# Kernel optimization log

Hardware: AMD Instinct MI355X
Metric: run time of the kernel (lower is better)

Reference implementation:

```python
import jax, jax.numpy as jnp
import numpy as np

D, H, E, TAU = 1024, 2048, 8, 0.1
X_SHAPE = (2, 2048, D)
N = X_SHAPE[0] * X_SHAPE[1]


def setup_inputs() -> dict:
    key = jax.random.key(0)
    ks = jax.random.split(key, 12)
    s_in = 1.0 / np.sqrt(D)
    s_hid = 1.0 / np.sqrt(H)
    return {
        "x": jax.random.normal(ks[0], X_SHAPE, jnp.float32),
        "gumbel_u": jax.random.uniform(ks[1], (N, E), jnp.float32, 1e-6, 1.0 - 1e-6),
        "eps": jax.random.normal(ks[2], (N, E, D), jnp.float32),
        "Wg1": jax.random.normal(ks[3], (D, H), jnp.float32) * s_in,
        "bg1": jnp.zeros((H,), jnp.float32),
        "Wg2": jax.random.normal(ks[4], (H, E), jnp.float32) * s_hid,
        "bg2": jnp.zeros((E,), jnp.float32),
        "Wm1": jax.random.normal(ks[5], (E, D, H), jnp.float32) * s_in,
        "bm1": jnp.zeros((E, H), jnp.float32),
        "Wm2": jax.random.normal(ks[6], (E, H, D), jnp.float32) * s_hid,
        "bm2": jnp.zeros((E, D), jnp.float32),
        "Wv1": jax.random.normal(ks[7], (E, D, H), jnp.float32) * s_in,
        "bv1": jnp.zeros((E, H), jnp.float32),
        "Wv2": jax.random.normal(ks[8], (E, H, D), jnp.float32) * s_hid,
        "bv2": jnp.zeros((E, D), jnp.float32),
    }


def reference(x, gumbel_u, eps, Wg1, bg1, Wg2, bg2, Wm1, bm1, Wm2, bm2, Wv1, bv1, Wv2, bv2):
    orig_shape = x.shape
    xf = x.reshape(-1, D)  # [N, D]

    # Gate: Linear -> ReLU -> Linear, then soft Gumbel-Softmax
    gate_logits = jax.nn.relu(xf @ Wg1 + bg1) @ Wg2 + bg2  # [N, E]
    gumbel = -jnp.log(-jnp.log(gumbel_u))
    w = jax.nn.softmax((gate_logits + gumbel) / TAU, axis=-1)  # [N, E]

    # Per-expert 2-layer MLPs, batched over the expert axis as grouped GEMMs
    hm = jax.nn.relu(jnp.einsum("nd,edh->neh", xf, Wm1) + bm1)
    mus = jnp.einsum("neh,ehd->ned", hm, Wm2) + bm2  # [N, E, D]
    hv = jax.nn.relu(jnp.einsum("nd,edh->neh", xf, Wv1) + bv1)
    logvars = jnp.einsum("neh,ehd->ned", hv, Wv2) + bv2  # [N, E, D]

    # Reparameterized sample per expert, then gate-weighted sum over experts
    samples = mus + eps * jnp.exp(0.5 * logvars)  # [N, E, D]
    out = jnp.einsum("ne,ned->nd", w, samples)  # [N, D]
    return out.reshape(orig_shape)
```

## Files before the change

kernel.cpp:

```cpp
#include <hip/hip_runtime.h>


typedef _Float16 f16x8 __attribute__((ext_vector_type(8)));
typedef float    f32x4 __attribute__((ext_vector_type(4)));

__device__ __forceinline__ void async_copy16(const void* g, void* l) {
  __builtin_amdgcn_global_load_lds(
      (const __attribute__((address_space(1))) void*)g,
      (__attribute__((address_space(3))) void*)l, 16, 0, 0);
}


__global__ __launch_bounds__(256) void split_x_kernel(
    const float* __restrict__ x, _Float16* __restrict__ Ax) {
  int idx = blockIdx.x * 256 + threadIdx.x;
  int m = idx >> 10, k = idx & 1023;
  float v = x[idx];
  _Float16 hi = (_Float16)v;
  _Float16 lo = (_Float16)(v - (float)hi);
  _Float16* row = Ax + (size_t)m * 3072;
  row[k] = hi;
  row[k + 1024] = hi;
  row[k + 2048] = lo;
}

__global__ __launch_bounds__(256) void split_transpose_wg1_kernel(
    const float* __restrict__ in, _Float16* __restrict__ out) {
  __shared__ float tile[64][65];
  int kb = blockIdx.y * 64, nb = blockIdx.x * 64;
  int c = threadIdx.x & 63, r0 = threadIdx.x >> 6;
#pragma unroll
  for (int i = 0; i < 16; ++i) {
    int r = r0 + i * 4;
    tile[r][c] = in[(size_t)(kb + r) * 2048 + nb + c];
  }
  __syncthreads();
#pragma unroll
  for (int i = 0; i < 16; ++i) {
    int rn = r0 + i * 4;
    float v = tile[c][rn];
    _Float16 hi = (_Float16)v;
    _Float16 lo = (_Float16)(v - (float)hi);
    _Float16* row = out + (size_t)(nb + rn) * 3072 + kb;
    row[c] = hi;
    row[c + 1024] = lo;
    row[c + 2048] = hi;
  }
}

__global__ __launch_bounds__(256) void transpose_f32_to_f16(
    const float* __restrict__ in, _Float16* __restrict__ out, int K, int N) {
  __shared__ float tile[64][65];
  size_t zo = (size_t)blockIdx.z * K * N;
  int kb = blockIdx.y * 64, nb = blockIdx.x * 64;
  int c = threadIdx.x & 63, r0 = threadIdx.x >> 6;
  const float* ip = in + zo + (size_t)kb * N + nb;
#pragma unroll
  for (int i = 0; i < 16; ++i) {
    int r = r0 + i * 4;
    tile[r][c] = ip[(size_t)r * N + c];
  }
  __syncthreads();
  _Float16* op = out + zo + (size_t)nb * K + kb;
#pragma unroll
  for (int i = 0; i < 16; ++i) {
    int rn = r0 + i * 4;
    op[(size_t)rn * K + c] = (_Float16)tile[c][rn];
  }
}

__global__ __launch_bounds__(256) void zero_out_kernel(float4* __restrict__ p) {
  p[blockIdx.x * 256 + threadIdx.x] = float4{0.f, 0.f, 0.f, 0.f};
}

__global__ __launch_bounds__(256) void gate_gemm1_kernel(
    const _Float16* __restrict__ A, const _Float16* __restrict__ Bt,
    float* __restrict__ C, const float* __restrict__ bias) {
  __shared__ _Float16 As[128 * 32];
  __shared__ _Float16 Bs[128 * 32];
  const int tid = threadIdx.x, lane = tid & 63, wid = tid >> 6;
  const int m0 = blockIdx.y * 128, n0 = blockIdx.x * 128;
  const int wm = (wid >> 1) * 64, wn = (wid & 1) * 64;
  const int lanelo = lane & 15, laneq = lane >> 4;
  const int K = 3072, lda = 3072, ldc = 2048;
  f32x4 acc[4][4] = {};

  const int c0 = wid * 128 + lane, c1 = c0 + 64;
  const int ra0 = c0 >> 2, ca0 = (c0 & 3) * 8;
  const int ra1 = c1 >> 2, ca1 = (c1 & 3) * 8;
  _Float16* ldsA0 = As + (wid * 128 + 0) * 8;
  _Float16* ldsA1 = As + (wid * 128 + 64) * 8;
  _Float16* ldsB0 = Bs + (wid * 128 + 0) * 8;
  _Float16* ldsB1 = Bs + (wid * 128 + 64) * 8;
  const _Float16* Arow0 = A + (size_t)(m0 + ra0) * lda + ca0;
  const _Float16* Arow1 = A + (size_t)(m0 + ra1) * lda + ca1;
  const _Float16* Brow0 = Bt + (size_t)(n0 + ra0) * K + ca0;
  const _Float16* Brow1 = Bt + (size_t)(n0 + ra1) * K + ca1;

  for (int k0 = 0; k0 < K; k0 += 32) {
    async_copy16(Arow0 + k0, ldsA0);
    async_copy16(Arow1 + k0, ldsA1);
    async_copy16(Brow0 + k0, ldsB0);
    async_copy16(Brow1 + k0, ldsB1);
    __syncthreads();
    f16x8 a[4], b[4];
#pragma unroll
    for (int i = 0; i < 4; ++i)
      a[i] = *reinterpret_cast<const f16x8*>(
          &As[(wm + i * 16 + lanelo) * 32 + laneq * 8]);
#pragma unroll
    for (int j = 0; j < 4; ++j)
      b[j] = *reinterpret_cast<const f16x8*>(
          &Bs[(wn + j * 16 + lanelo) * 32 + laneq * 8]);
#pragma unroll
    for (int i = 0; i < 4; ++i)
#pragma unroll
      for (int j = 0; j < 4; ++j)
        acc[i][j] =
            __builtin_amdgcn_mfma_f32_16x16x32_f16(a[i], b[j], acc[i][j], 0, 0, 0);
    __syncthreads();
  }

#pragma unroll
  for (int j = 0; j < 4; ++j) {
    const int n = n0 + wn + j * 16 + lanelo;
    const float bn = bias[n];
#pragma unroll
    for (int i = 0; i < 4; ++i) {
#pragma unroll
      for (int r = 0; r < 4; ++r) {
        const int m = m0 + wm + i * 16 + laneq * 4 + r;
        float v = acc[i][j][r] + bn;
        C[(size_t)m * ldc + n] = v > 0.f ? v : 0.f;
      }
    }
  }
}

__global__ __launch_bounds__(256) void expert_gemm1_kernel(
    const _Float16* __restrict__ A, const _Float16* __restrict__ W1t,
    _Float16* __restrict__ hm, _Float16* __restrict__ hv,
    const float* __restrict__ bm1, const float* __restrict__ bv1) {
  __shared__ _Float16 As[128 * 32];
  __shared__ _Float16 Bs[128 * 32];
  const int tid = threadIdx.x, lane = tid & 63, wid = tid >> 6;
  const int s = blockIdx.z & 1, e = blockIdx.z >> 1;
  const _Float16* __restrict__ Bt = W1t + (size_t)(s * 8 + e) * 2048 * 1024;
  _Float16* __restrict__ C = (s ? hv : hm) + (size_t)e * 4096 * 2048;
  const float* __restrict__ bias = (s ? bv1 : bm1) + e * 2048;
  const int m0 = blockIdx.y * 128, n0 = blockIdx.x * 128;
  const int wm = (wid >> 1) * 64, wn = (wid & 1) * 64;
  const int lanelo = lane & 15, laneq = lane >> 4;
  const int K = 1024, lda = 3072, ldc = 2048;
  f32x4 acc[4][4] = {};

  const int c0 = wid * 128 + lane, c1 = c0 + 64;
  const int ra0 = c0 >> 2, ca0 = (c0 & 3) * 8;
  const int ra1 = c1 >> 2, ca1 = (c1 & 3) * 8;
  _Float16* ldsA0 = As + (wid * 128 + 0) * 8;
  _Float16* ldsA1 = As + (wid * 128 + 64) * 8;
  _Float16* ldsB0 = Bs + (wid * 128 + 0) * 8;
  _Float16* ldsB1 = Bs + (wid * 128 + 64) * 8;
  const _Float16* Arow0 = A + (size_t)(m0 + ra0) * lda + ca0;
  const _Float16* Arow1 = A + (size_t)(m0 + ra1) * lda + ca1;
  const _Float16* Brow0 = Bt + (size_t)(n0 + ra0) * K + ca0;
  const _Float16* Brow1 = Bt + (size_t)(n0 + ra1) * K + ca1;

  for (int k0 = 0; k0 < K; k0 += 32) {
    async_copy16(Arow0 + k0, ldsA0);
    async_copy16(Arow1 + k0, ldsA1);
    async_copy16(Brow0 + k0, ldsB0);
    async_copy16(Brow1 + k0, ldsB1);
    __syncthreads();
    f16x8 a[4], b[4];
#pragma unroll
    for (int i = 0; i < 4; ++i)
      a[i] = *reinterpret_cast<const f16x8*>(
          &As[(wm + i * 16 + lanelo) * 32 + laneq * 8]);
#pragma unroll
    for (int j = 0; j < 4; ++j)
      b[j] = *reinterpret_cast<const f16x8*>(
          &Bs[(wn + j * 16 + lanelo) * 32 + laneq * 8]);
#pragma unroll
    for (int i = 0; i < 4; ++i)
#pragma unroll
      for (int j = 0; j < 4; ++j)
        acc[i][j] =
            __builtin_amdgcn_mfma_f32_16x16x32_f16(a[i], b[j], acc[i][j], 0, 0, 0);
    __syncthreads();
  }

#pragma unroll
  for (int j = 0; j < 4; ++j) {
    const int n = n0 + wn + j * 16 + lanelo;
    const float bn = bias[n];
#pragma unroll
    for (int i = 0; i < 4; ++i) {
#pragma unroll
      for (int r = 0; r < 4; ++r) {
        const int m = m0 + wm + i * 16 + laneq * 4 + r;
        float v = acc[i][j][r] + bn;
        C[(size_t)m * ldc + n] = (_Float16)(v > 0.f ? v : 0.f);
      }
    }
  }
}

__global__ __launch_bounds__(256) void gemm2_combine_kernel(
    const _Float16* __restrict__ hm, const _Float16* __restrict__ hv,
    const _Float16* __restrict__ W2t, const float* __restrict__ bm2,
    const float* __restrict__ bv2, const float* __restrict__ eps,
    const float* __restrict__ w, float* __restrict__ out) {
  __shared__ _Float16 As[128 * 32];
  __shared__ _Float16 Bs[128 * 32];
  const int tid = threadIdx.x, lane = tid & 63, wid = tid >> 6;
  const int s = blockIdx.z & 1, e = blockIdx.z >> 1;
  const _Float16* __restrict__ A = (s ? hv : hm) + (size_t)e * 4096 * 2048;
  const _Float16* __restrict__ Bt = W2t + (size_t)(s * 8 + e) * 1024 * 2048;
  const float* __restrict__ bias = (s ? bv2 : bm2) + e * 1024;
  const float* __restrict__ epsE = eps + e * 1024;
  const int m0 = blockIdx.y * 128, n0 = blockIdx.x * 128;
  const int wm = (wid >> 1) * 64, wn = (wid & 1) * 64;
  const int lanelo = lane & 15, laneq = lane >> 4;
  const int K = 2048, lda = 2048;
  f32x4 acc[4][4] = {};

  const int c0 = wid * 128 + lane, c1 = c0 + 64;
  const int ra0 = c0 >> 2, ca0 = (c0 & 3) * 8;
  const int ra1 = c1 >> 2, ca1 = (c1 & 3) * 8;
  _Float16* ldsA0 = As + (wid * 128 + 0) * 8;
  _Float16* ldsA1 = As + (wid * 128 + 64) * 8;
  _Float16* ldsB0 = Bs + (wid * 128 + 0) * 8;
  _Float16* ldsB1 = Bs + (wid * 128 + 64) * 8;
  const _Float16* Arow0 = A + (size_t)(m0 + ra0) * lda + ca0;
  const _Float16* Arow1 = A + (size_t)(m0 + ra1) * lda + ca1;
  const _Float16* Brow0 = Bt + (size_t)(n0 + ra0) * K + ca0;
  const _Float16* Brow1 = Bt + (size_t)(n0 + ra1) * K + ca1;

  for (int k0 = 0; k0 < K; k0 += 32) {
    async_copy16(Arow0 + k0, ldsA0);
    async_copy16(Arow1 + k0, ldsA1);
    async_copy16(Brow0 + k0, ldsB0);
    async_copy16(Brow1 + k0, ldsB1);
    __syncthreads();
    f16x8 a[4], b[4];
#pragma unroll
    for (int i = 0; i < 4; ++i)
      a[i] = *reinterpret_cast<const f16x8*>(
          &As[(wm + i * 16 + lanelo) * 32 + laneq * 8]);
#pragma unroll
    for (int j = 0; j < 4; ++j)
      b[j] = *reinterpret_cast<const f16x8*>(
          &Bs[(wn + j * 16 + lanelo) * 32 + laneq * 8]);
#pragma unroll
    for (int i = 0; i < 4; ++i)
#pragma unroll
      for (int j = 0; j < 4; ++j)
        acc[i][j] =
            __builtin_amdgcn_mfma_f32_16x16x32_f16(a[i], b[j], acc[i][j], 0, 0, 0);
    __syncthreads();
  }

#pragma unroll
  for (int i = 0; i < 4; ++i) {
#pragma unroll
    for (int r = 0; r < 4; ++r) {
      const int m = m0 + wm + i * 16 + laneq * 4 + r;
      const float wgt = w[(size_t)m * 8 + e];
      const float* erow = epsE + (size_t)m * 8192;
      float* orow = out + (size_t)m * 1024;
#pragma unroll
      for (int j = 0; j < 4; ++j) {
        const int d = n0 + wn + j * 16 + lanelo;
        const float t = acc[i][j][r] + bias[d];
        const float val =
            s ? wgt * erow[d] * __expf(0.5f * t) : wgt * t;
        unsafeAtomicAdd(&orow[d], val);
      }
    }
  }
}

__global__ __launch_bounds__(256) void gate_finish_kernel(
    const float* __restrict__ hg, const float* __restrict__ Wg2,
    const float* __restrict__ bg2, const float* __restrict__ gu,
    float* __restrict__ w) {
  const int lane = threadIdx.x & 63, wid = threadIdx.x >> 6;
  const int row = blockIdx.x * 4 + wid;
  const float* hrow = hg + (size_t)row * 2048;
  float acc[8] = {0.f, 0.f, 0.f, 0.f, 0.f, 0.f, 0.f, 0.f};
  for (int h = lane; h < 2048; h += 64) {
    const float hv = hrow[h];
    const float* wr = Wg2 + (size_t)h * 8;
#pragma unroll
    for (int e = 0; e < 8; ++e) acc[e] += hv * wr[e];
  }
#pragma unroll
  for (int off = 32; off > 0; off >>= 1) {
#pragma unroll
    for (int e = 0; e < 8; ++e) acc[e] += __shfl_down(acc[e], off);
  }
  if (lane == 0) {
    float z[8], zmax = -1e30f;
#pragma unroll
    for (int e = 0; e < 8; ++e) {
      const float u = gu[(size_t)row * 8 + e];
      const float g = -logf(-logf(u));
      z[e] = (acc[e] + bg2[e] + g) / 0.1f;
      zmax = fmaxf(zmax, z[e]);
    }
    float s = 0.f;
#pragma unroll
    for (int e = 0; e < 8; ++e) {
      z[e] = __expf(z[e] - zmax);
      s += z[e];
    }
    const float inv = 1.f / s;
#pragma unroll
    for (int e = 0; e < 8; ++e) w[(size_t)row * 8 + e] = z[e] * inv;
  }
}


extern "C" void kernel_launch(void* const* d_in, const int* in_sizes, int n_in,
                              void* d_out, int out_size, void* d_ws,
                              size_t ws_size, hipStream_t stream) {
  const float* x = (const float*)d_in[0];
  const float* gu = (const float*)d_in[1];
  const float* eps = (const float*)d_in[2];
  const float* Wg1 = (const float*)d_in[3];
  const float* bg1 = (const float*)d_in[4];
  const float* Wg2 = (const float*)d_in[5];
  const float* bg2 = (const float*)d_in[6];
  const float* Wm1 = (const float*)d_in[7];
  const float* bm1 = (const float*)d_in[8];
  const float* Wm2 = (const float*)d_in[9];
  const float* bm2 = (const float*)d_in[10];
  const float* Wv1 = (const float*)d_in[11];
  const float* bv1 = (const float*)d_in[12];
  const float* Wv2 = (const float*)d_in[13];
  const float* bv2 = (const float*)d_in[14];
  float* out = (float*)d_out;

  char* ws = (char*)d_ws;
  size_t off = 0;
  auto alloc = [&](size_t bytes) -> void* {
    void* p = ws + off;
    off = (off + bytes + 255) & ~(size_t)255;
    return p;
  };
  _Float16* Ax = (_Float16*)alloc(4096UL * 3072 * 2);
  _Float16* Wg1t = (_Float16*)alloc(2048UL * 3072 * 2);
  _Float16* W1t = (_Float16*)alloc(16UL * 2048 * 1024 * 2);
  _Float16* W2t = (_Float16*)alloc(16UL * 1024 * 2048 * 2);
  float* hg = (float*)alloc(4096UL * 2048 * 4);
  float* wbuf = (float*)alloc(4096UL * 8 * 4);
  _Float16* hm = (_Float16*)alloc(8UL * 4096 * 2048 * 2);
  _Float16* hv = (_Float16*)alloc(8UL * 4096 * 2048 * 2);

  zero_out_kernel<<<4096, 256, 0, stream>>>((float4*)out);
  split_x_kernel<<<4096 * 1024 / 256, 256, 0, stream>>>(x, Ax);
  split_transpose_wg1_kernel<<<dim3(2048 / 64, 1024 / 64), 256, 0, stream>>>(Wg1, Wg1t);
  transpose_f32_to_f16<<<dim3(2048 / 64, 1024 / 64, 8), 256, 0, stream>>>(
      Wm1, W1t, 1024, 2048);
  transpose_f32_to_f16<<<dim3(2048 / 64, 1024 / 64, 8), 256, 0, stream>>>(
      Wv1, W1t + 8UL * 2048 * 1024, 1024, 2048);
  transpose_f32_to_f16<<<dim3(1024 / 64, 2048 / 64, 8), 256, 0, stream>>>(
      Wm2, W2t, 2048, 1024);
  transpose_f32_to_f16<<<dim3(1024 / 64, 2048 / 64, 8), 256, 0, stream>>>(
      Wv2, W2t + 8UL * 1024 * 2048, 2048, 1024);

  gate_gemm1_kernel<<<dim3(2048 / 128, 4096 / 128), 256, 0, stream>>>(
      Ax, Wg1t, hg, bg1);
  gate_finish_kernel<<<4096 / 4, 256, 0, stream>>>(hg, Wg2, bg2, gu, wbuf);

  expert_gemm1_kernel<<<dim3(2048 / 128, 4096 / 128, 16), 256, 0, stream>>>(
      Ax, W1t, hm, hv, bm1, bv1);
  gemm2_combine_kernel<<<dim3(1024 / 128, 4096 / 128, 16), 256, 0, stream>>>(
      hm, hv, W2t, bm2, bv2, eps, wbuf, out);
}
```

Baseline: 1.410 ms.

## Fuse mu/logvar expert GEMMs to share A tiles and halve output atomics

Expert GEMM1 now computes both the mu and logvar hidden tiles in one block, loading the shared x tile once and keeping two accumulator sets. GEMM2 runs the logvar GEMM first, folds eps*exp(0.5*logvar)+mu-bias into the accumulator, then continues accumulating the mu GEMM on top, so each output element gets a single atomic add per expert instead of two. The LDS write offsets are also simplified to c0*8. This cuts A-tile traffic and atomics at the cost of higher register pressure (two accumulator sets, launch_bounds 256,2) and half as many blocks per launch.

```diff
diff --git a/kernel.cpp b/kernel.cpp
--- a/kernel.cpp
+++ b/kernel.cpp
@@ -88,10 +88,10 @@
   const int c0 = wid * 128 + lane, c1 = c0 + 64;
   const int ra0 = c0 >> 2, ca0 = (c0 & 3) * 8;
   const int ra1 = c1 >> 2, ca1 = (c1 & 3) * 8;
-  _Float16* ldsA0 = As + (wid * 128 + 0) * 8;
-  _Float16* ldsA1 = As + (wid * 128 + 64) * 8;
-  _Float16* ldsB0 = Bs + (wid * 128 + 0) * 8;
-  _Float16* ldsB1 = Bs + (wid * 128 + 64) * 8;
+  _Float16* ldsA0 = As + c0 * 8;
+  _Float16* ldsA1 = As + c1 * 8;
+  _Float16* ldsB0 = Bs + c0 * 8;
+  _Float16* ldsB1 = Bs + c1 * 8;
   const _Float16* Arow0 = A + (size_t)(m0 + ra0) * lda + ca0;
   const _Float16* Arow1 = A + (size_t)(m0 + ra1) * lda + ca1;
   const _Float16* Brow0 = Bt + (size_t)(n0 + ra0) * K + ca0;
@@ -137,40 +137,51 @@
   }
 }
 
-__global__ __launch_bounds__(256) void expert_gemm1_kernel(
+__global__ __launch_bounds__(256, 2) void expert_gemm1_kernel(
     const _Float16* __restrict__ A, const _Float16* __restrict__ W1t,
     _Float16* __restrict__ hm, _Float16* __restrict__ hv,
     const float* __restrict__ bm1, const float* __restrict__ bv1) {
   __shared__ _Float16 As[128 * 32];
-  __shared__ _Float16 Bs[128 * 32];
+  __shared__ _Float16 Bms[128 * 32];
+  __shared__ _Float16 Bvs[128 * 32];
   const int tid = threadIdx.x, lane = tid & 63, wid = tid >> 6;
-  const int s = blockIdx.z & 1, e = blockIdx.z >> 1;
-  const _Float16* __restrict__ Bt = W1t + (size_t)(s * 8 + e) * 2048 * 1024;
-  _Float16* __restrict__ C = (s ? hv : hm) + (size_t)e * 4096 * 2048;
-  const float* __restrict__ bias = (s ? bv1 : bm1) + e * 2048;
+  const int e = blockIdx.z;
+  const _Float16* __restrict__ Btm = W1t + (size_t)e * 2048 * 1024;
+  const _Float16* __restrict__ Btv = W1t + (size_t)(8 + e) * 2048 * 1024;
+  _Float16* __restrict__ Cm = hm + (size_t)e * 4096 * 2048;
+  _Float16* __restrict__ Cv = hv + (size_t)e * 4096 * 2048;
+  const float* __restrict__ bm = bm1 + e * 2048;
+  const float* __restrict__ bv = bv1 + e * 2048;
   const int m0 = blockIdx.y * 128, n0 = blockIdx.x * 128;
   const int wm = (wid >> 1) * 64, wn = (wid & 1) * 64;
   const int lanelo = lane & 15, laneq = lane >> 4;
   const int K = 1024, lda = 3072, ldc = 2048;
-  f32x4 acc[4][4] = {};
+  f32x4 accm[4][4] = {};
+  f32x4 accv[4][4] = {};
 
   const int c0 = wid * 128 + lane, c1 = c0 + 64;
   const int ra0 = c0 >> 2, ca0 = (c0 & 3) * 8;
   const int ra1 = c1 >> 2, ca1 = (c1 & 3) * 8;
-  _Float16* ldsA0 = As + (wid * 128 + 0) * 8;
-  _Float16* ldsA1 = As + (wid * 128 + 64) * 8;
-  _Float16* ldsB0 = Bs + (wid * 128 + 0) * 8;
-  _Float16* ldsB1 = Bs + (wid * 128 + 64) * 8;
+  _Float16* ldsA0 = As + c0 * 8;
+  _Float16* ldsA1 = As + c1 * 8;
+  _Float16* ldsBm0 = Bms + c0 * 8;
+  _Float16* ldsBm1 = Bms + c1 * 8;
+  _Float16* ldsBv0 = Bvs + c0 * 8;
+  _Float16* ldsBv1 = Bvs + c1 * 8;
   const _Float16* Arow0 = A + (size_t)(m0 + ra0) * lda + ca0;
   const _Float16* Arow1 = A + (size_t)(m0 + ra1) * lda + ca1;
-  const _Float16* Brow0 = Bt + (size_t)(n0 + ra0) * K + ca0;
-  const _Float16* Brow1 = Bt + (size_t)(n0 + ra1) * K + ca1;
+  const _Float16* Bmrow0 = Btm + (size_t)(n0 + ra0) * K + ca0;
+  const _Float16* Bmrow1 = Btm + (size_t)(n0 + ra1) * K + ca1;
+  const _Float16* Bvrow0 = Btv + (size_t)(n0 + ra0) * K + ca0;
+  const _Float16* Bvrow1 = Btv + (size_t)(n0 + ra1) * K + ca1;
 
   for (int k0 = 0; k0 < K; k0 += 32) {
     async_copy16(Arow0 + k0, ldsA0);
     async_copy16(Arow1 + k0, ldsA1);
-    async_copy16(Brow0 + k0, ldsB0);
-    async_copy16(Brow1 + k0, ldsB1);
+    async_copy16(Bmrow0 + k0, ldsBm0);
+    async_copy16(Bmrow1 + k0, ldsBm1);
+    async_copy16(Bvrow0 + k0, ldsBv0);
+    async_copy16(Bvrow1 + k0, ldsBv1);
     __syncthreads();
     f16x8 a[4], b[4];
 #pragma unroll
@@ -180,27 +191,39 @@
 #pragma unroll
     for (int j = 0; j < 4; ++j)
       b[j] = *reinterpret_cast<const f16x8*>(
-          &Bs[(wn + j * 16 + lanelo) * 32 + laneq * 8]);
+          &Bms[(wn + j * 16 + lanelo) * 32 + laneq * 8]);
 #pragma unroll
     for (int i = 0; i < 4; ++i)
 #pragma unroll
       for (int j = 0; j < 4; ++j)
-        acc[i][j] =
-            __builtin_amdgcn_mfma_f32_16x16x32_f16(a[i], b[j], acc[i][j], 0, 0, 0);
+        accm[i][j] =
+            __builtin_amdgcn_mfma_f32_16x16x32_f16(a[i], b[j], accm[i][j], 0, 0, 0);
+#pragma unroll
+    for (int j = 0; j < 4; ++j)
+      b[j] = *reinterpret_cast<const f16x8*>(
+          &Bvs[(wn + j * 16 + lanelo) * 32 + laneq * 8]);
+#pragma unroll
+    for (int i = 0; i < 4; ++i)
+#pragma unroll
+      for (int j = 0; j < 4; ++j)
+        accv[i][j] =
+            __builtin_amdgcn_mfma_f32_16x16x32_f16(a[i], b[j], accv[i][j], 0, 0, 0);
     __syncthreads();
   }
 
 #pragma unroll
   for (int j = 0; j < 4; ++j) {
     const int n = n0 + wn + j * 16 + lanelo;
-    const float bn = bias[n];
+    const float bmn = bm[n], bvn = bv[n];
 #pragma unroll
     for (int i = 0; i < 4; ++i) {
 #pragma unroll
       for (int r = 0; r < 4; ++r) {
         const int m = m0 + wm + i * 16 + laneq * 4 + r;
-        float v = acc[i][j][r] + bn;
-        C[(size_t)m * ldc + n] = (_Float16)(v > 0.f ? v : 0.f);
+        float vm = accm[i][j][r] + bmn;
+        float vv = accv[i][j][r] + bvn;
+        Cm[(size_t)m * ldc + n] = (_Float16)(vm > 0.f ? vm : 0.f);
+        Cv[(size_t)m * ldc + n] = (_Float16)(vv > 0.f ? vv : 0.f);
       }
     }
   }
@@ -214,11 +237,13 @@
   __shared__ _Float16 As[128 * 32];
   __shared__ _Float16 Bs[128 * 32];
   const int tid = threadIdx.x, lane = tid & 63, wid = tid >> 6;
-  const int s = blockIdx.z & 1, e = blockIdx.z >> 1;
-  const _Float16* __restrict__ A = (s ? hv : hm) + (size_t)e * 4096 * 2048;
-  const _Float16* __restrict__ Bt = W2t + (size_t)(s * 8 + e) * 1024 * 2048;
-  const float* __restrict__ bias = (s ? bv2 : bm2) + e * 1024;
-  const float* __restrict__ epsE = eps + e * 1024;
+  const int e = blockIdx.z;
+  const _Float16* __restrict__ Am = hm + (size_t)e * 4096 * 2048;
+  const _Float16* __restrict__ Av = hv + (size_t)e * 4096 * 2048;
+  const _Float16* __restrict__ Btm = W2t + (size_t)e * 1024 * 2048;
+  const _Float16* __restrict__ Btv = W2t + (size_t)(8 + e) * 1024 * 2048;
+  const float* __restrict__ bmb = bm2 + e * 1024;
+  const float* __restrict__ bvb = bv2 + e * 1024;
   const int m0 = blockIdx.y * 128, n0 = blockIdx.x * 128;
   const int wm = (wid >> 1) * 64, wn = (wid & 1) * 64;
   const int lanelo = lane & 15, laneq = lane >> 4;
@@ -228,37 +253,89 @@
   const int c0 = wid * 128 + lane, c1 = c0 + 64;
   const int ra0 = c0 >> 2, ca0 = (c0 & 3) * 8;
   const int ra1 = c1 >> 2, ca1 = (c1 & 3) * 8;
-  _Float16* ldsA0 = As + (wid * 128 + 0) * 8;
-  _Float16* ldsA1 = As + (wid * 128 + 64) * 8;
-  _Float16* ldsB0 = Bs + (wid * 128 + 0) * 8;
-  _Float16* ldsB1 = Bs + (wid * 128 + 64) * 8;
-  const _Float16* Arow0 = A + (size_t)(m0 + ra0) * lda + ca0;
-  const _Float16* Arow1 = A + (size_t)(m0 + ra1) * lda + ca1;
-  const _Float16* Brow0 = Bt + (size_t)(n0 + ra0) * K + ca0;
-  const _Float16* Brow1 = Bt + (size_t)(n0 + ra1) * K + ca1;
-
-  for (int k0 = 0; k0 < K; k0 += 32) {
-    async_copy16(Arow0 + k0, ldsA0);
-    async_copy16(Arow1 + k0, ldsA1);
-    async_copy16(Brow0 + k0, ldsB0);
-    async_copy16(Brow1 + k0, ldsB1);
-    __syncthreads();
-    f16x8 a[4], b[4];
-#pragma unroll
-    for (int i = 0; i < 4; ++i)
-      a[i] = *reinterpret_cast<const f16x8*>(
-          &As[(wm + i * 16 + lanelo) * 32 + laneq * 8]);
-#pragma unroll
-    for (int j = 0; j < 4; ++j)
-      b[j] = *reinterpret_cast<const f16x8*>(
-          &Bs[(wn + j * 16 + lanelo) * 32 + laneq * 8]);
-#pragma unroll
-    for (int i = 0; i < 4; ++i)
+  _Float16* ldsA0 = As + c0 * 8;
+  _Float16* ldsA1 = As + c1 * 8;
+  _Float16* ldsB0 = Bs + c0 * 8;
+  _Float16* ldsB1 = Bs + c1 * 8;
+  const size_t aoff0 = (size_t)(m0 + ra0) * lda + ca0;
+  const size_t aoff1 = (size_t)(m0 + ra1) * lda + ca1;
+  const size_t boff0 = (size_t)(n0 + ra0) * K + ca0;
+  const size_t boff1 = (size_t)(n0 + ra1) * K + ca1;
+
+  {
+    const _Float16* Arow0 = Av + aoff0;
+    const _Float16* Arow1 = Av + aoff1;
+    const _Float16* Brow0 = Btv + boff0;
+    const _Float16* Brow1 = Btv + boff1;
+    for (int k0 = 0; k0 < K; k0 += 32) {
+      async_copy16(Arow0 + k0, ldsA0);
+      async_copy16(Arow1 + k0, ldsA1);
+      async_copy16(Brow0 + k0, ldsB0);
+      async_copy16(Brow1 + k0, ldsB1);
+      __syncthreads();
+      f16x8 a[4], b[4];
+#pragma unroll
+      for (int i = 0; i < 4; ++i)
+        a[i] = *reinterpret_cast<const f16x8*>(
+            &As[(wm + i * 16 + lanelo) * 32 + laneq * 8]);
 #pragma unroll
       for (int j = 0; j < 4; ++j)
-        acc[i][j] =
-            __builtin_amdgcn_mfma_f32_16x16x32_f16(a[i], b[j], acc[i][j], 0, 0, 0);
-    __syncthreads();
+        b[j] = *reinterpret_cast<const f16x8*>(
+            &Bs[(wn + j * 16 + lanelo) * 32 + laneq * 8]);
+#pragma unroll
+      for (int i = 0; i < 4; ++i)
+#pragma unroll
+        for (int j = 0; j < 4; ++j)
+          acc[i][j] =
+              __builtin_amdgcn_mfma_f32_16x16x32_f16(a[i], b[j], acc[i][j], 0, 0, 0);
+      __syncthreads();
+    }
+  }
+
+#pragma unroll
+  for (int j = 0; j < 4; ++j) {
+    const int d = n0 + wn + j * 16 + lanelo;
+    const float bvd = bvb[d];
+    const float bmd = bmb[d];
+#pragma unroll
+    for (int i = 0; i < 4; ++i) {
+#pragma unroll
+      for (int r = 0; r < 4; ++r) {
+        const int m = m0 + wm + i * 16 + laneq * 4 + r;
+        const float ev = eps[(size_t)m * 8192 + e * 1024 + d];
+        acc[i][j][r] = ev * __expf(0.5f * (acc[i][j][r] + bvd)) + bmd;
+      }
+    }
+  }
+
+  {
+    const _Float16* Arow0 = Am + aoff0;
+    const _Float16* Arow1 = Am + aoff1;
+    const _Float16* Brow0 = Btm + boff0;
+    const _Float16* Brow1 = Btm + boff1;
+    for (int k0 = 0; k0 < K; k0 += 32) {
+      async_copy16(Arow0 + k0, ldsA0);
+      async_copy16(Arow1 + k0, ldsA1);
+      async_copy16(Brow0 + k0, ldsB0);
+      async_copy16(Brow1 + k0, ldsB1);
+      __syncthreads();
+      f16x8 a[4], b[4];
+#pragma unroll
+      for (int i = 0; i < 4; ++i)
+        a[i] = *reinterpret_cast<const f16x8*>(
+            &As[(wm + i * 16 + lanelo) * 32 + laneq * 8]);
+#pragma unroll
+      for (int j = 0; j < 4; ++j)
+        b[j] = *reinterpret_cast<const f16x8*>(
+            &Bs[(wn + j * 16 + lanelo) * 32 + laneq * 8]);
+#pragma unroll
+      for (int i = 0; i < 4; ++i)
+#pragma unroll
+        for (int j = 0; j < 4; ++j)
+          acc[i][j] =
+              __builtin_amdgcn_mfma_f32_16x16x32_f16(a[i], b[j], acc[i][j], 0, 0, 0);
+      __syncthreads();
+    }
   }
 
 #pragma unroll
@@ -267,15 +344,11 @@
     for (int r = 0; r < 4; ++r) {
       const int m = m0 + wm + i * 16 + laneq * 4 + r;
       const float wgt = w[(size_t)m * 8 + e];
-      const float* erow = epsE + (size_t)m * 8192;
       float* orow = out + (size_t)m * 1024;
 #pragma unroll
       for (int j = 0; j < 4; ++j) {
         const int d = n0 + wn + j * 16 + lanelo;
-        const float t = acc[i][j][r] + bias[d];
-        const float val =
-            s ? wgt * erow[d] * __expf(0.5f * t) : wgt * t;
-        unsafeAtomicAdd(&orow[d], val);
+        unsafeAtomicAdd(&orow[d], wgt * acc[i][j][r]);
       }
     }
   }
@@ -374,8 +447,8 @@
       Ax, Wg1t, hg, bg1);
   gate_finish_kernel<<<4096 / 4, 256, 0, stream>>>(hg, Wg2, bg2, gu, wbuf);
 
-  expert_gemm1_kernel<<<dim3(2048 / 128, 4096 / 128, 16), 256, 0, stream>>>(
+  expert_gemm1_kernel<<<dim3(2048 / 128, 4096 / 128, 8), 256, 0, stream>>>(
       Ax, W1t, hm, hv, bm1, bv1);
-  gemm2_combine_kernel<<<dim3(1024 / 128, 4096 / 128, 16), 256, 0, stream>>>(
+  gemm2_combine_kernel<<<dim3(1024 / 128, 4096 / 128, 8), 256, 0, stream>>>(
       hm, hv, W2t, bm2, bv2, eps, wbuf, out);
 }
```

New measurement: 1.384 ms. About the same (-1.9%).

## Replace GEMMs with 256x256 double-buffered swizzled MFMA tiles and fuse mu/logvar combine

Applied to the files above, without the earlier changes.

Replaces the three 128x128 single-buffered GEMM kernels with a shared 256x256-tile, 512-thread routine. It uses 128KB of dynamic LDS, double buffering with async global-to-LDS copies, XOR-swizzled layout, split barriers and setprio around the MFMA bursts. The combine kernel now computes the logvar and mu GEMMs for each expert in one block and keeps the sample in registers, which halves the atomic adds to the output. This trades larger tiles and register pressure (two blocks per CU requested) for more data reuse and less LDS stall and atomic traffic.

```diff
diff --git a/kernel.cpp b/kernel.cpp
--- a/kernel.cpp
+++ b/kernel.cpp
@@ -9,6 +9,8 @@
       (const __attribute__((address_space(1))) void*)g,
       (__attribute__((address_space(3))) void*)l, 16, 0, 0);
 }
+
+#define MFMA16(a_, b_, c_) __builtin_amdgcn_mfma_f32_16x16x32_f16(a_, b_, c_, 0, 0, 0)
 
 
 __global__ __launch_bounds__(256) void split_x_kernel(
@@ -73,212 +75,271 @@
   p[blockIdx.x * 256 + threadIdx.x] = float4{0.f, 0.f, 0.f, 0.f};
 }
 
-__global__ __launch_bounds__(256) void gate_gemm1_kernel(
+__device__ __forceinline__ void gemm256_acc(
+    const _Float16* __restrict__ Abase, const int lda,
+    const _Float16* __restrict__ Bbase, const int ldb,
+    const int NT, _Float16* lds, f32x4 (&acc)[8][4]) {
+  const int tid = threadIdx.x;
+  const int lane = tid & 63, wid = tid >> 6;
+  const int wm = wid >> 2, wn = wid & 3;
+  const int lanelo = lane & 15, laneq = lane >> 4;
+  const int colp0 = (laneq * 8) ^ ((lanelo & 7) << 3);
+  const int rowoffA = (wm * 128 + lanelo) * 64;
+  const int rowoffB = (wn * 64 + lanelo) * 64;
+
+  _Float16* const As0 = lds;
+  _Float16* const As1 = lds + 16384;
+  _Float16* const Bs0 = lds + 32768;
+  _Float16* const Bs1 = lds + 49152;
+
+  const int sr = tid >> 3;
+  const int sc = ((tid & 7) ^ (sr & 7)) << 3;
+  const size_t goffA = (size_t)sr * lda + sc;
+  const size_t goffB = (size_t)sr * ldb + sc;
+  const size_t rowsA64 = (size_t)64 * lda;
+  const size_t rowsB64 = (size_t)64 * ldb;
+  const int tid8 = tid * 8;
+
+#define STAGE_A(dstbuf, kp, hf)                                  \
+  do {                                                           \
+    const _Float16* g_ = (kp) + (size_t)(hf)*2 * rowsA64 + goffA;\
+    _Float16* d_ = (dstbuf) + (hf)*8192 + tid8;                  \
+    async_copy16(g_, d_);                                        \
+    async_copy16(g_ + rowsA64, d_ + 4096);                       \
+  } while (0)
+#define STAGE_B(dstbuf, kp, hf)                                  \
+  do {                                                           \
+    const _Float16* g_ = (kp) + (size_t)(hf)*2 * rowsB64 + goffB;\
+    _Float16* d_ = (dstbuf) + (hf)*8192 + tid8;                  \
+    async_copy16(g_, d_);                                        \
+    async_copy16(g_ + rowsB64, d_ + 4096);                       \
+  } while (0)
+#define BARRIER() asm volatile("s_barrier" ::: "memory")
+
+  const _Float16* aN = Abase + 64;
+  const _Float16* bN = Bbase + 128;
+
+  STAGE_A(As0, Abase, 0);
+  STAGE_A(As0, Abase, 1);
+  STAGE_B(Bs0, Bbase, 0);
+  STAGE_B(Bs0, Bbase, 1);
+  STAGE_B(Bs1, Bbase + 64, 0);
+  STAGE_B(Bs1, Bbase + 64, 1);
+  asm volatile("s_waitcnt vmcnt(4)" ::: "memory");
+  BARRIER();
+
+  for (int kt = 0; kt < NT; ++kt) {
+    _Float16* const bufA = (kt & 1) ? As1 : As0;
+    _Float16* const bufB = (kt & 1) ? Bs1 : Bs0;
+    _Float16* const nxtA = (kt & 1) ? As0 : As1;
+    const _Float16* const rA0 = bufA + rowoffA + colp0;
+    const _Float16* const rA1 = bufA + rowoffA + (colp0 ^ 32);
+    const _Float16* const rB0 = bufB + rowoffB + colp0;
+    const _Float16* const rB1 = bufB + rowoffB + (colp0 ^ 32);
+    const bool st1 = (kt + 1 < NT), st2 = (kt + 2 < NT);
+    f16x8 a[4][2], b[4][2];
+
+#pragma unroll
+    for (int i = 0; i < 4; ++i) {
+      a[i][0] = *(const f16x8*)(rA0 + i * 1024);
+      a[i][1] = *(const f16x8*)(rA1 + i * 1024);
+    }
+#pragma unroll
+    for (int j = 0; j < 2; ++j) {
+      b[j][0] = *(const f16x8*)(rB0 + j * 1024);
+      b[j][1] = *(const f16x8*)(rB1 + j * 1024);
+    }
+    if (st1) STAGE_A(nxtA, aN, 0);
+    BARRIER();
+    __builtin_amdgcn_sched_barrier(0);
+    __builtin_amdgcn_s_setprio(1);
+#pragma unroll
+    for (int i = 0; i < 4; ++i)
+#pragma unroll
+      for (int j = 0; j < 2; ++j) {
+        acc[i][j] = MFMA16(a[i][0], b[j][0], acc[i][j]);
+        acc[i][j] = MFMA16(a[i][1], b[j][1], acc[i][j]);
+      }
+    __builtin_amdgcn_s_setprio(0);
+    __builtin_amdgcn_sched_barrier(0);
+    BARRIER();
+
+#pragma unroll
+    for (int j = 0; j < 2; ++j) {
+      b[2 + j][0] = *(const f16x8*)(rB0 + (2 + j) * 1024);
+      b[2 + j][1] = *(const f16x8*)(rB1 + (2 + j) * 1024);
+    }
+    if (st1) STAGE_A(nxtA, aN, 1);
+    BARRIER();
+    __builtin_amdgcn_sched_barrier(0);
+    __builtin_amdgcn_s_setprio(1);
+#pragma unroll
+    for (int i = 0; i < 4; ++i)
+#pragma unroll
+      for (int j = 0; j < 2; ++j) {
+        acc[i][2 + j] = MFMA16(a[i][0], b[2 + j][0], acc[i][2 + j]);
+        acc[i][2 + j] = MFMA16(a[i][1], b[2 + j][1], acc[i][2 + j]);
+      }
+    __builtin_amdgcn_s_setprio(0);
+    __builtin_amdgcn_sched_barrier(0);
+    BARRIER();
+
+#pragma unroll
+    for (int i = 0; i < 4; ++i) {
+      a[i][0] = *(const f16x8*)(rA0 + 4096 + i * 1024);
+      a[i][1] = *(const f16x8*)(rA1 + 4096 + i * 1024);
+    }
+    if (st2) STAGE_B(bufB, bN, 0);
+    BARRIER();
+    __builtin_amdgcn_sched_barrier(0);
+    __builtin_amdgcn_s_setprio(1);
+#pragma unroll
+    for (int i = 0; i < 4; ++i)
+#pragma unroll
+      for (int j = 0; j < 2; ++j) {
+        acc[4 + i][j] = MFMA16(a[i][0], b[j][0], acc[4 + i][j]);
+        acc[4 + i][j] = MFMA16(a[i][1], b[j][1], acc[4 + i][j]);
+      }
+    __builtin_amdgcn_s_setprio(0);
+    __builtin_amdgcn_sched_barrier(0);
+    BARRIER();
+
+    if (st2) STAGE_B(bufB, bN, 1);
+    BARRIER();
+    __builtin_amdgcn_sched_barrier(0);
+    __builtin_amdgcn_s_setprio(1);
+#pragma unroll
+    for (int i = 0; i < 4; ++i)
+#pragma unroll
+      for (int j = 0; j < 2; ++j) {
+        acc[4 + i][2 + j] = MFMA16(a[i][0], b[2 + j][0], acc[4 + i][2 + j]);
+        acc[4 + i][2 + j] = MFMA16(a[i][1], b[2 + j][1], acc[4 + i][2 + j]);
+      }
+    __builtin_amdgcn_s_setprio(0);
+    __builtin_amdgcn_sched_barrier(0);
+    if (st2) {
+      asm volatile("s_waitcnt vmcnt(4)" ::: "memory");
+    } else {
+      asm volatile("s_waitcnt vmcnt(0)" ::: "memory");
+    }
+    BARRIER();
+
+    aN += 64;
+    bN += 64;
+  }
+#undef STAGE_A
+#undef STAGE_B
+#undef BARRIER
+}
+
+__global__ __launch_bounds__(512, 2) void gate_gemm1_256(
     const _Float16* __restrict__ A, const _Float16* __restrict__ Bt,
     float* __restrict__ C, const float* __restrict__ bias) {
-  __shared__ _Float16 As[128 * 32];
-  __shared__ _Float16 Bs[128 * 32];
+  extern __shared__ _Float16 lds[];
+  const int m0 = blockIdx.y * 256, n0 = blockIdx.x * 256;
+  f32x4 acc[8][4] = {};
+  gemm256_acc(A + (size_t)m0 * 3072, 3072, Bt + (size_t)n0 * 3072, 3072, 48,
+              lds, acc);
   const int tid = threadIdx.x, lane = tid & 63, wid = tid >> 6;
-  const int m0 = blockIdx.y * 128, n0 = blockIdx.x * 128;
-  const int wm = (wid >> 1) * 64, wn = (wid & 1) * 64;
+  const int wm = wid >> 2, wn = wid & 3;
   const int lanelo = lane & 15, laneq = lane >> 4;
-  const int K = 3072, lda = 3072, ldc = 2048;
-  f32x4 acc[4][4] = {};
-
-  const int c0 = wid * 128 + lane, c1 = c0 + 64;
-  const int ra0 = c0 >> 2, ca0 = (c0 & 3) * 8;
-  const int ra1 = c1 >> 2, ca1 = (c1 & 3) * 8;
-  _Float16* ldsA0 = As + (wid * 128 + 0) * 8;
-  _Float16* ldsA1 = As + (wid * 128 + 64) * 8;
-  _Float16* ldsB0 = Bs + (wid * 128 + 0) * 8;
-  _Float16* ldsB1 = Bs + (wid * 128 + 64) * 8;
-  const _Float16* Arow0 = A + (size_t)(m0 + ra0) * lda + ca0;
-  const _Float16* Arow1 = A + (size_t)(m0 + ra1) * lda + ca1;
-  const _Float16* Brow0 = Bt + (size_t)(n0 + ra0) * K + ca0;
-  const _Float16* Brow1 = Bt + (size_t)(n0 + ra1) * K + ca1;
-
-  for (int k0 = 0; k0 < K; k0 += 32) {
-    async_copy16(Arow0 + k0, ldsA0);
-    async_copy16(Arow1 + k0, ldsA1);
-    async_copy16(Brow0 + k0, ldsB0);
-    async_copy16(Brow1 + k0, ldsB1);
-    __syncthreads();
-    f16x8 a[4], b[4];
-#pragma unroll
-    for (int i = 0; i < 4; ++i)
-      a[i] = *reinterpret_cast<const f16x8*>(
-          &As[(wm + i * 16 + lanelo) * 32 + laneq * 8]);
-#pragma unroll
-    for (int j = 0; j < 4; ++j)
-      b[j] = *reinterpret_cast<const f16x8*>(
-          &Bs[(wn + j * 16 + lanelo) * 32 + laneq * 8]);
-#pragma unroll
-    for (int i = 0; i < 4; ++i)
-#pragma unroll
-      for (int j = 0; j < 4; ++j)
-        acc[i][j] =
-            __builtin_amdgcn_mfma_f32_16x16x32_f16(a[i], b[j], acc[i][j], 0, 0, 0);
-    __syncthreads();
-  }
-
-#pragma unroll
-  for (int j = 0; j < 4; ++j) {
-    const int n = n0 + wn + j * 16 + lanelo;
+#pragma unroll
+  for (int nf = 0; nf < 4; ++nf) {
+    const int n = n0 + wn * 64 + nf * 16 + lanelo;
     const float bn = bias[n];
 #pragma unroll
-    for (int i = 0; i < 4; ++i) {
+    for (int mf = 0; mf < 8; ++mf)
 #pragma unroll
       for (int r = 0; r < 4; ++r) {
-        const int m = m0 + wm + i * 16 + laneq * 4 + r;
-        float v = acc[i][j][r] + bn;
-        C[(size_t)m * ldc + n] = v > 0.f ? v : 0.f;
-      }
-    }
-  }
-}
-
-__global__ __launch_bounds__(256) void expert_gemm1_kernel(
+        const int m = m0 + wm * 128 + mf * 16 + laneq * 4 + r;
+        float v = acc[mf][nf][r] + bn;
+        C[(size_t)m * 2048 + n] = v > 0.f ? v : 0.f;
+      }
+  }
+}
+
+__global__ __launch_bounds__(512, 2) void expert_gemm1_256(
     const _Float16* __restrict__ A, const _Float16* __restrict__ W1t,
     _Float16* __restrict__ hm, _Float16* __restrict__ hv,
     const float* __restrict__ bm1, const float* __restrict__ bv1) {
-  __shared__ _Float16 As[128 * 32];
-  __shared__ _Float16 Bs[128 * 32];
-  const int tid = threadIdx.x, lane = tid & 63, wid = tid >> 6;
-  const int s = blockIdx.z & 1, e = blockIdx.z >> 1;
-  const _Float16* __restrict__ Bt = W1t + (size_t)(s * 8 + e) * 2048 * 1024;
+  extern __shared__ _Float16 lds[];
+  const int z = blockIdx.z, e = z & 7, s = z >> 3;
+  const _Float16* __restrict__ Bt = W1t + (size_t)z * 2048 * 1024;
   _Float16* __restrict__ C = (s ? hv : hm) + (size_t)e * 4096 * 2048;
   const float* __restrict__ bias = (s ? bv1 : bm1) + e * 2048;
-  const int m0 = blockIdx.y * 128, n0 = blockIdx.x * 128;
-  const int wm = (wid >> 1) * 64, wn = (wid & 1) * 64;
+  const int m0 = blockIdx.y * 256, n0 = blockIdx.x * 256;
+  f32x4 acc[8][4] = {};
+  gemm256_acc(A + (size_t)m0 * 3072, 3072, Bt + (size_t)n0 * 1024, 1024, 16,
+              lds, acc);
+  const int tid = threadIdx.x, lane = tid & 63, wid = tid >> 6;
+  const int wm = wid >> 2, wn = wid & 3;
   const int lanelo = lane & 15, laneq = lane >> 4;
-  const int K = 1024, lda = 3072, ldc = 2048;
-  f32x4 acc[4][4] = {};
-
-  const int c0 = wid * 128 + lane, c1 = c0 + 64;
-  const int ra0 = c0 >> 2, ca0 = (c0 & 3) * 8;
-  const int ra1 = c1 >> 2, ca1 = (c1 & 3) * 8;
-  _Float16* ldsA0 = As + (wid * 128 + 0) * 8;
-  _Float16* ldsA1 = As + (wid * 128 + 64) * 8;
-  _Float16* ldsB0 = Bs + (wid * 128 + 0) * 8;
-  _Float16* ldsB1 = Bs + (wid * 128 + 64) * 8;
-  const _Float16* Arow0 = A + (size_t)(m0 + ra0) * lda + ca0;
-  const _Float16* Arow1 = A + (size_t)(m0 + ra1) * lda + ca1;
-  const _Float16* Brow0 = Bt + (size_t)(n0 + ra0) * K + ca0;
-  const _Float16* Brow1 = Bt + (size_t)(n0 + ra1) * K + ca1;
-
-  for (int k0 = 0; k0 < K; k0 += 32) {
-    async_copy16(Arow0 + k0, ldsA0);
-    async_copy16(Arow1 + k0, ldsA1);
-    async_copy16(Brow0 + k0, ldsB0);
-    async_copy16(Brow1 + k0, ldsB1);
-    __syncthreads();
-    f16x8 a[4], b[4];
-#pragma unroll
-    for (int i = 0; i < 4; ++i)
-      a[i] = *reinterpret_cast<const f16x8*>(
-          &As[(wm + i * 16 + lanelo) * 32 + laneq * 8]);
-#pragma unroll
-    for (int j = 0; j < 4; ++j)
-      b[j] = *reinterpret_cast<const f16x8*>(
-          &Bs[(wn + j * 16 + lanelo) * 32 + laneq * 8]);
-#pragma unroll
-    for (int i = 0; i < 4; ++i)
-#pragma unroll
-      for (int j = 0; j < 4; ++j)
-        acc[i][j] =
-            __builtin_amdgcn_mfma_f32_16x16x32_f16(a[i], b[j], acc[i][j], 0, 0, 0);
-    __syncthreads();
-  }
-
-#pragma unroll
-  for (int j = 0; j < 4; ++j) {
-    const int n = n0 + wn + j * 16 + lanelo;
+#pragma unroll
+  for (int nf = 0; nf < 4; ++nf) {
+    const int n = n0 + wn * 64 + nf * 16 + lanelo;
     const float bn = bias[n];
 #pragma unroll
-    for (int i = 0; i < 4; ++i) {
+    for (int mf = 0; mf < 8; ++mf)
 #pragma unroll
       for (int r = 0; r < 4; ++r) {
-        const int m = m0 + wm + i * 16 + laneq * 4 + r;
-        float v = acc[i][j][r] + bn;
-        C[(size_t)m * ldc + n] = (_Float16)(v > 0.f ? v : 0.f);
-      }
-    }
-  }
-}
-
-__global__ __launch_bounds__(256) void gemm2_combine_kernel(
+        const int m = m0 + wm * 128 + mf * 16 + laneq * 4 + r;
+        float v = acc[mf][nf][r] + bn;
+        C[(size_t)m * 2048 + n] = (_Float16)(v > 0.f ? v : 0.f);
+      }
+  }
+}
+
+__global__ __launch_bounds__(512, 2) void gemm2_combine_256(
     const _Float16* __restrict__ hm, const _Float16* __restrict__ hv,
     const _Float16* __restrict__ W2t, const float* __restrict__ bm2,
     const float* __restrict__ bv2, const float* __restrict__ eps,
     const float* __restrict__ w, float* __restrict__ out) {
-  __shared__ _Float16 As[128 * 32];
-  __shared__ _Float16 Bs[128 * 32];
+  extern __shared__ _Float16 lds[];
+  const int e = blockIdx.z;
+  const _Float16* __restrict__ Am = hm + (size_t)e * 4096 * 2048;
+  const _Float16* __restrict__ Av = hv + (size_t)e * 4096 * 2048;
+  const _Float16* __restrict__ Btm = W2t + (size_t)e * 1024 * 2048;
+  const _Float16* __restrict__ Btv = W2t + (size_t)(8 + e) * 1024 * 2048;
+  const float* __restrict__ bmb = bm2 + e * 1024;
+  const float* __restrict__ bvb = bv2 + e * 1024;
+  const int m0 = blockIdx.y * 256, n0 = blockIdx.x * 256;
   const int tid = threadIdx.x, lane = tid & 63, wid = tid >> 6;
-  const int s = blockIdx.z & 1, e = blockIdx.z >> 1;
-  const _Float16* __restrict__ A = (s ? hv : hm) + (size_t)e * 4096 * 2048;
-  const _Float16* __restrict__ Bt = W2t + (size_t)(s * 8 + e) * 1024 * 2048;
-  const float* __restrict__ bias = (s ? bv2 : bm2) + e * 1024;
-  const float* __restrict__ epsE = eps + e * 1024;
-  const int m0 = blockIdx.y * 128, n0 = blockIdx.x * 128;
-  const int wm = (wid >> 1) * 64, wn = (wid & 1) * 64;
+  const int wm = wid >> 2, wn = wid & 3;
   const int lanelo = lane & 15, laneq = lane >> 4;
-  const int K = 2048, lda = 2048;
-  f32x4 acc[4][4] = {};
-
-  const int c0 = wid * 128 + lane, c1 = c0 + 64;
-  const int ra0 = c0 >> 2, ca0 = (c0 & 3) * 8;
-  const int ra1 = c1 >> 2, ca1 = (c1 & 3) * 8;
-  _Float16* ldsA0 = As + (wid * 128 + 0) * 8;
-  _Float16* ldsA1 = As + (wid * 128 + 64) * 8;
-  _Float16* ldsB0 = Bs + (wid * 128 + 0) * 8;
-  _Float16* ldsB1 = Bs + (wid * 128 + 64) * 8;
-  const _Float16* Arow0 = A + (size_t)(m0 + ra0) * lda + ca0;
-  const _Float16* Arow1 = A + (size_t)(m0 + ra1) * lda + ca1;
-  const _Float16* Brow0 = Bt + (size_t)(n0 + ra0) * K + ca0;
-  const _Float16* Brow1 = Bt + (size_t)(n0 + ra1) * K + ca1;
-
-  for (int k0 = 0; k0 < K; k0 += 32) {
-    async_copy16(Arow0 + k0, ldsA0);
-    async_copy16(Arow1 + k0, ldsA1);
-    async_copy16(Brow0 + k0, ldsB0);
-    async_copy16(Brow1 + k0, ldsB1);
-    __syncthreads();
-    f16x8 a[4], b[4];
-#pragma unroll
-    for (int i = 0; i < 4; ++i)
-      a[i] = *reinterpret_cast<const f16x8*>(
-          &As[(wm + i * 16 + lanelo) * 32 + laneq * 8]);
-#pragma unroll
-    for (int j = 0; j < 4; ++j)
-      b[j] = *reinterpret_cast<const f16x8*>(
-          &Bs[(wn + j * 16 + lanelo) * 32 + laneq * 8]);
-#pragma unroll
-    for (int i = 0; i < 4; ++i)
-#pragma unroll
-      for (int j = 0; j < 4; ++j)
-        acc[i][j] =
-            __builtin_amdgcn_mfma_f32_16x16x32_f16(a[i], b[j], acc[i][j], 0, 0, 0);
-    __syncthreads();
-  }
-
-#pragma unroll
-  for (int i = 0; i < 4; ++i) {
+
+  f32x4 acc[8][4] = {};
+  gemm256_acc(Av + (size_t)m0 * 2048, 2048, Btv + (size_t)n0 * 2048, 2048, 32,
+              lds, acc);
+#pragma unroll
+  for (int nf = 0; nf < 4; ++nf) {
+    const int d = n0 + wn * 64 + nf * 16 + lanelo;
+    const float bvd = bvb[d];
+    const float bmd = bmb[d];
+#pragma unroll
+    for (int mf = 0; mf < 8; ++mf)
+#pragma unroll
+      for (int r = 0; r < 4; ++r) {
+        const int m = m0 + wm * 128 + mf * 16 + laneq * 4 + r;
+        const float ev = eps[(size_t)m * 8192 + e * 1024 + d];
+        acc[mf][nf][r] = ev * __expf(0.5f * (acc[mf][nf][r] + bvd)) + bmd;
+      }
+  }
+  asm volatile("s_barrier" ::: "memory");
+  gemm256_acc(Am + (size_t)m0 * 2048, 2048, Btm + (size_t)n0 * 2048, 2048, 32,
+              lds, acc);
+#pragma unroll
+  for (int mf = 0; mf < 8; ++mf)
 #pragma unroll
     for (int r = 0; r < 4; ++r) {
-      const int m = m0 + wm + i * 16 + laneq * 4 + r;
+      const int m = m0 + wm * 128 + mf * 16 + laneq * 4 + r;
       const float wgt = w[(size_t)m * 8 + e];
-      const float* erow = epsE + (size_t)m * 8192;
       float* orow = out + (size_t)m * 1024;
 #pragma unroll
-      for (int j = 0; j < 4; ++j) {
-        const int d = n0 + wn + j * 16 + lanelo;
-        const float t = acc[i][j][r] + bias[d];
-        const float val =
-            s ? wgt * erow[d] * __expf(0.5f * t) : wgt * t;
-        unsafeAtomicAdd(&orow[d], val);
-      }
-    }
-  }
+      for (int nf = 0; nf < 4; ++nf) {
+        const int d = n0 + wn * 64 + nf * 16 + lanelo;
+        unsafeAtomicAdd(&orow[d], wgt * acc[mf][nf][r]);
+      }
+    }
 }
 
 __global__ __launch_bounds__(256) void gate_finish_kernel(
@@ -342,6 +403,20 @@
   const float* bv2 = (const float*)d_in[14];
   float* out = (float*)d_out;
 
+  static bool attr_done = false;
+  if (!attr_done) {
+    (void)hipFuncSetAttribute((const void*)gate_gemm1_256,
+                              hipFuncAttributeMaxDynamicSharedMemorySize,
+                              131072);
+    (void)hipFuncSetAttribute((const void*)expert_gemm1_256,
+                              hipFuncAttributeMaxDynamicSharedMemorySize,
+                              131072);
+    (void)hipFuncSetAttribute((const void*)gemm2_combine_256,
+                              hipFuncAttributeMaxDynamicSharedMemorySize,
+                              131072);
+    attr_done = true;
+  }
+
   char* ws = (char*)d_ws;
   size_t off = 0;
   auto alloc = [&](size_t bytes) -> void* {
@@ -370,12 +445,12 @@
   transpose_f32_to_f16<<<dim3(1024 / 64, 2048 / 64, 8), 256, 0, stream>>>(
       Wv2, W2t + 8UL * 1024 * 2048, 2048, 1024);
 
-  gate_gemm1_kernel<<<dim3(2048 / 128, 4096 / 128), 256, 0, stream>>>(
+  gate_gemm1_256<<<dim3(2048 / 256, 4096 / 256), 512, 131072, stream>>>(
       Ax, Wg1t, hg, bg1);
   gate_finish_kernel<<<4096 / 4, 256, 0, stream>>>(hg, Wg2, bg2, gu, wbuf);
 
-  expert_gemm1_kernel<<<dim3(2048 / 128, 4096 / 128, 16), 256, 0, stream>>>(
+  expert_gemm1_256<<<dim3(2048 / 256, 4096 / 256, 16), 512, 131072, stream>>>(
       Ax, W1t, hm, hv, bm1, bv1);
-  gemm2_combine_kernel<<<dim3(1024 / 128, 4096 / 128, 16), 256, 0, stream>>>(
+  gemm2_combine_256<<<dim3(1024 / 256, 4096 / 256, 8), 512, 131072, stream>>>(
       hm, hv, W2t, bm2, bv2, eps, wbuf, out);
 }
```

Measured after the change: 1.170 ms. 17.0% less time.
